# Optimization experiments

Hardware: AMD Instinct MI355X
Metric: run time of the kernel (lower is better)

## Reference

```python
import jax, jax.numpy as jnp
import numpy as np
from jax import lax

B, T, H = 4096, 2048, 32


def setup_inputs() -> dict:
    key = jax.random.key(0)
    ks = jax.random.split(key, 10)
    s = 1.0 / np.sqrt(H)  # PyTorch LSTM/Linear init scale
    x = jax.random.normal(ks[0], (B, T, 1), dtype=jnp.float32)
    lengths = jax.random.randint(ks[1], (B,), 1, T + 1, dtype=jnp.int32)
    u = lambda k, shape, sc: jax.random.uniform(k, shape, jnp.float32, -sc, sc)
    return {
        "x": x,
        "lengths": lengths,
        # backward-direction LSTM weights (only h_n[-1] is used by the head)
        "w_ih": u(ks[2], (4 * H, 1), s),
        "w_hh": u(ks[3], (4 * H, H), s),
        "b_ih": u(ks[4], (4 * H,), s),
        "b_hh": u(ks[5], (4 * H,), s),
        "fc_w": u(ks[6], (64, H), 1.0 / np.sqrt(H)),
        "fc_b": u(ks[7], (64,), 1.0 / np.sqrt(H)),
        "fc2_w": u(ks[8], (1, 64), 1.0 / np.sqrt(64)),
        "fc2_b": u(ks[9], (1,), 1.0 / np.sqrt(64)),
    }


def _backward_lstm_final(x, lengths, w_ih, w_hh, b_ih, b_hh):
    """Final hidden state of the backward direction of a packed BiLSTM.

    The backward direction reads each sequence from t=len-1 down to t=0 with
    zero initial state. Equivalently: scan padded x in reverse time order and
    only update (h, c) where t < length (packed-sequence semantics).
    """
    Bv, Tv, _ = x.shape
    ts = jnp.arange(Tv - 1, -1, -1)                       # reversed time indices
    xs_t = jnp.transpose(x[:, ::-1, :], (1, 0, 2))        # [T, B, 1]
    mask_t = ts[:, None] < lengths[None, :]               # [T, B]

    def step(carry, inp):
        h, c = carry
        xt, m = inp                                        # [B,1], [B]
        gates = xt @ w_ih.T + b_ih + h @ w_hh.T + b_hh     # [B, 4H]
        i, f, g, o = jnp.split(gates, 4, axis=-1)
        i = jax.nn.sigmoid(i)
        f = jax.nn.sigmoid(f)
        g = jnp.tanh(g)
        o = jax.nn.sigmoid(o)
        c_new = f * c + i * g
        h_new = o * jnp.tanh(c_new)
        mm = m[:, None]
        return (jnp.where(mm, h_new, h), jnp.where(mm, c_new, c)), None

    h0 = jnp.zeros((Bv, H), dtype=x.dtype)
    c0 = jnp.zeros((Bv, H), dtype=x.dtype)
    (h_n, _), _ = lax.scan(step, (h0, c0), (xs_t, mask_t))
    return h_n                                             # [B, H]


def reference(x, lengths, w_ih, w_hh, b_ih, b_hh, fc_w, fc_b, fc2_w, fc2_b):
    h_n = _backward_lstm_final(x, lengths, w_ih, w_hh, b_ih, b_hh)
    out = jax.nn.elu(h_n @ fc_w.T + fc_b)                  # [B, 64]
    out = jax.nn.sigmoid(out @ fc2_w.T + fc2_b)            # [B, 1]
    return out
```

## Files before the change

kernel.cpp:

```cpp
#include <hip/hip_runtime.h>

constexpr int BB = 4096;
constexpr int TT = 2048;
constexpr int HH = 32;
constexpr int GE = 16;

typedef float v4f __attribute__((ext_vector_type(4)));
typedef float f32x4 __attribute__((ext_vector_type(4)));
typedef _Float16 f16x8 __attribute__((ext_vector_type(8)));
typedef _Float16 v2h __attribute__((ext_vector_type(2)));
typedef _Float16 v8h __attribute__((ext_vector_type(8)));

__device__ __forceinline__ float fexp2(float x) { return __builtin_amdgcn_exp2f(x); }
__device__ __forceinline__ float frcp(float x)  { return __builtin_amdgcn_rcpf(x); }
__device__ __forceinline__ float fsigmoid(float x) {
    return frcp(1.0f + fexp2(x * -1.4426950408889634f));
}
__device__ __forceinline__ float felu(float x) {
    return x > 0.0f ? x : (fexp2(x * 1.4426950408889634f) - 1.0f);
}

__global__ void sort_by_len_kernel(const int* __restrict__ lengths, int* __restrict__ perm) {
    __shared__ int hist[TT];
    __shared__ int csum[256];
    const int tid = threadIdx.x;
    for (int i = tid; i < TT; i += 256) hist[i] = 0;
    __syncthreads();
    for (int i = tid; i < BB; i += 256) atomicAdd(&hist[TT - lengths[i]], 1);
    __syncthreads();
    const int base = tid * 8;
    int loc[8];
    int s = 0;
#pragma unroll
    for (int j = 0; j < 8; ++j) { loc[j] = hist[base + j]; s += loc[j]; }
    csum[tid] = s;
    __syncthreads();
    for (int off = 1; off < 256; off <<= 1) {
        int v = (tid >= off) ? csum[tid - off] : 0;
        __syncthreads();
        csum[tid] += v;
        __syncthreads();
    }
    int run = csum[tid] - s;
#pragma unroll
    for (int j = 0; j < 8; ++j) { int t = loc[j]; hist[base + j] = run; run += t; }
    __syncthreads();
    for (int i = tid; i < BB; i += 256) {
        int pos = atomicAdd(&hist[TT - lengths[i]], 1);
        perm[pos] = i;
    }
}

__global__ __attribute__((amdgpu_flat_work_group_size(256, 256)))
void lstm_kernel(const float* __restrict__ x, const int* __restrict__ lengths,
                 const float* __restrict__ w_ih, const float* __restrict__ w_hh,
                 const float* __restrict__ b_ih, const float* __restrict__ b_hh,
                 const float* __restrict__ fc_w, const float* __restrict__ fc_b,
                 const float* __restrict__ fc2_w, const float* __restrict__ fc2_b,
                 float* __restrict__ out, const int* __restrict__ perm) {
    __shared__ __align__(16) _Float16 hb[2][GE][40];
    __shared__ __align__(16) float xls[GE][68];
    __shared__ int barr[GE];
    __shared__ int Llds[GE];
    __shared__ int maxLs;

    const int tid  = threadIdx.x;
    const int wv   = tid >> 6;
    const int lane = tid & 63;
    const int lg   = lane >> 4;
    const int e    = lane & 15;

    const int g = blockIdx.x;
    if (tid < GE) {
        const int b = perm ? perm[GE * g + tid] : (GE * g + tid);
        barr[tid] = b;
        Llds[tid] = lengths[b];
    }
    for (int i = tid; i < 2 * GE * 40; i += 256) ((_Float16*)hb)[i] = (_Float16)0.0f;
    __syncthreads();
    if (tid == 0) {
        int m = 0;
        for (int i = 0; i < GE; ++i) m = max(m, Llds[i]);
        maxLs = m;
    }
    __syncthreads();
    const int maxL = maxLs;
    const int Lme  = Llds[e];

    const float NL2E = -1.4426950408889634f;

    const int r = lane & 15;
    const int sgate = r & 3;
    const int qq = r >> 2;
    const float asc = (sgate == 2) ? 2.0f * NL2E : NL2E;
    f16x8 afr[2];
#pragma unroll
    for (int m = 0; m < 2; ++m) {
        const int u = 8 * wv + 2 * qq + m;
        const int wrow = sgate * 32 + u;
        const v4f* wp = reinterpret_cast<const v4f*>(w_hh + wrow * 32 + 8 * lg);
        const v4f wa = wp[0], wb = wp[1];
        afr[m] = (f16x8){(_Float16)(wa.x * asc), (_Float16)(wa.y * asc),
                         (_Float16)(wa.z * asc), (_Float16)(wa.w * asc),
                         (_Float16)(wb.x * asc), (_Float16)(wb.y * asc),
                         (_Float16)(wb.z * asc), (_Float16)(wb.w * asc)};
    }
    float wih_[2][4], bs_[2][4];
#pragma unroll
    for (int m = 0; m < 2; ++m) {
        const int u = 8 * wv + 2 * lg + m;
#pragma unroll
        for (int i = 0; i < 4; ++i) {
            const float scd = (i == 2) ? 2.0f * NL2E : NL2E;
            wih_[m][i] = w_ih[i * 32 + u] * scd;
            bs_[m][i]  = (b_ih[i * 32 + u] + b_hh[i * 32 + u]) * scd;
        }
    }

    float c0 = 0.0f, c1 = 0.0f;
    int p = 0;
    const int hoff = 8 * wv + 2 * lg;

    for (int s = maxL - 1; s >= 0; --s) {
        if (s == maxL - 1 || (s & 63) == 63) {
            const int tb = s & ~63;
            const int es = tid >> 4, j4 = (tid & 15) * 4;
            const float* xp = x + (size_t)barr[es] * TT + tb + j4;
            *reinterpret_cast<v4f*>(&xls[es][j4]) = *reinterpret_cast<const v4f*>(xp);
            __syncthreads();
        }
        const f16x8 bf = *reinterpret_cast<const f16x8*>(&hb[p][e][lg * 8]);
        const float xe = xls[e][s & 63];
        f32x4 C0, C1;
#pragma unroll
        for (int i = 0; i < 4; ++i) {
            C0[i] = fmaf(wih_[0][i], xe, bs_[0][i]);
            C1[i] = fmaf(wih_[1][i], xe, bs_[1][i]);
        }
        const f32x4 D0 = __builtin_amdgcn_mfma_f32_16x16x32_f16(afr[0], bf, C0, 0, 0, 0);
        const f32x4 D1 = __builtin_amdgcn_mfma_f32_16x16x32_f16(afr[1], bf, C1, 0, 0, 0);
        const bool act = (s < Lme);

        float h0, h1;
        {
            const float Ei = fexp2(D0[0]), Ef = fexp2(D0[1]);
            const float Eg = fexp2(D0[2]), Eo = fexp2(D0[3]);
            const float R1 = frcp((1.0f + Ei) * (1.0f + Eg));
            const float ig = (1.0f - Eg) * R1;
            const float R2 = frcp((1.0f + Ef) * (1.0f + Eo));
            const float sf = (1.0f + Eo) * R2;
            const float so = (1.0f + Ef) * R2;
            const float cn = fmaf(sf, c0, ig);
            c0 = act ? cn : c0;
            const float tc = 1.0f - 2.0f * frcp(1.0f + fexp2(c0 * 2.8853900817779268f));
            h0 = act ? (so * tc) : 0.0f;
        }
        {
            const float Ei = fexp2(D1[0]), Ef = fexp2(D1[1]);
            const float Eg = fexp2(D1[2]), Eo = fexp2(D1[3]);
            const float R1 = frcp((1.0f + Ei) * (1.0f + Eg));
            const float ig = (1.0f - Eg) * R1;
            const float R2 = frcp((1.0f + Ef) * (1.0f + Eo));
            const float sf = (1.0f + Eo) * R2;
            const float so = (1.0f + Ef) * R2;
            const float cn = fmaf(sf, c1, ig);
            c1 = act ? cn : c1;
            const float tc = 1.0f - 2.0f * frcp(1.0f + fexp2(c1 * 2.8853900817779268f));
            h1 = act ? (so * tc) : 0.0f;
        }
        const v2h pk = {(_Float16)h0, (_Float16)h1};
        *reinterpret_cast<v2h*>(&hb[p ^ 1][e][hoff]) = pk;
        __syncthreads();
        p ^= 1;
    }

    for (int e2 = 4 * wv; e2 < 4 * wv + 4; ++e2) {
        float hf[32];
        const v8h* hp8 = reinterpret_cast<const v8h*>(&hb[p][e2][0]);
#pragma unroll
        for (int q4 = 0; q4 < 4; ++q4) {
            const v8h hh = hp8[q4];
#pragma unroll
            for (int j = 0; j < 8; ++j) hf[8 * q4 + j] = (float)hh[j];
        }
        float a = fc_b[lane];
        const v4f* fp = reinterpret_cast<const v4f*>(fc_w + lane * 32);
#pragma unroll
        for (int q4 = 0; q4 < 8; ++q4) {
            const v4f f = fp[q4];
            a = fmaf(f.x, hf[4 * q4 + 0], a);
            a = fmaf(f.y, hf[4 * q4 + 1], a);
            a = fmaf(f.z, hf[4 * q4 + 2], a);
            a = fmaf(f.w, hf[4 * q4 + 3], a);
        }
        float partial = felu(a) * fc2_w[lane];
#pragma unroll
        for (int m = 32; m >= 1; m >>= 1) partial += __shfl_xor(partial, m, 64);
        if (lane == 0) out[barr[e2]] = fsigmoid(partial + fc2_b[0]);
    }
}

extern "C" void kernel_launch(void* const* d_in, const int* in_sizes, int n_in,
                              void* d_out, int out_size, void* d_ws, size_t ws_size,
                              hipStream_t stream) {
    const float* x       = (const float*)d_in[0];
    const int*   lengths = (const int*)d_in[1];
    const float* w_ih    = (const float*)d_in[2];
    const float* w_hh    = (const float*)d_in[3];
    const float* b_ih    = (const float*)d_in[4];
    const float* b_hh    = (const float*)d_in[5];
    const float* fc_w    = (const float*)d_in[6];
    const float* fc_b    = (const float*)d_in[7];
    const float* fc2_w   = (const float*)d_in[8];
    const float* fc2_b   = (const float*)d_in[9];
    float* out = (float*)d_out;

    int* perm = nullptr;
    if (ws_size >= (size_t)BB * sizeof(int)) {
        perm = (int*)d_ws;
        hipLaunchKernelGGL(sort_by_len_kernel, dim3(1), dim3(256), 0, stream, lengths, perm);
    }
    hipLaunchKernelGGL(lstm_kernel, dim3(BB / GE), dim3(256), 0, stream,
                       x, lengths, w_ih, w_hh, b_ih, b_hh,
                       fc_w, fc_b, fc2_w, fc2_b, out, perm);
}
```

Before: 676.6 us.

## Split LSTM hidden units across eight waves, one MFMA per wave per step

Doubles the workgroup from 256 to 512 threads so each wave owns four hidden units instead of eight. Each wave issues one MFMA and one set of gate activations per timestep instead of two, which shortens the per-step serial critical path. In exchange, every step's block-wide barrier now synchronises twice as many waves, and each block uses more CUs' worth of wave slots, which lowers how many blocks can run at once.

```diff
diff --git a/kernel.cpp b/kernel.cpp
--- a/kernel.cpp
+++ b/kernel.cpp
@@ -5,10 +5,10 @@
 constexpr int HH = 32;
 constexpr int GE = 16;
 
+typedef float v2f __attribute__((ext_vector_type(2)));
 typedef float v4f __attribute__((ext_vector_type(4)));
 typedef float f32x4 __attribute__((ext_vector_type(4)));
 typedef _Float16 f16x8 __attribute__((ext_vector_type(8)));
-typedef _Float16 v2h __attribute__((ext_vector_type(2)));
 typedef _Float16 v8h __attribute__((ext_vector_type(8)));
 
 __device__ __forceinline__ float fexp2(float x) { return __builtin_amdgcn_exp2f(x); }
@@ -51,7 +51,7 @@
     }
 }
 
-__global__ __attribute__((amdgpu_flat_work_group_size(256, 256)))
+__global__ __attribute__((amdgpu_flat_work_group_size(512, 512)))
 void lstm_kernel(const float* __restrict__ x, const int* __restrict__ lengths,
                  const float* __restrict__ w_ih, const float* __restrict__ w_hh,
                  const float* __restrict__ b_ih, const float* __restrict__ b_hh,
@@ -76,7 +76,7 @@
         barr[tid] = b;
         Llds[tid] = lengths[b];
     }
-    for (int i = tid; i < 2 * GE * 40; i += 256) ((_Float16*)hb)[i] = (_Float16)0.0f;
+    for (int i = tid; i < 2 * GE * 40; i += 512) ((_Float16*)hb)[i] = (_Float16)0.0f;
     __syncthreads();
     if (tid == 0) {
         int m = 0;
@@ -89,92 +89,65 @@
 
     const float NL2E = -1.4426950408889634f;
 
-    const int r = lane & 15;
-    const int sgate = r & 3;
-    const int qq = r >> 2;
-    const float asc = (sgate == 2) ? 2.0f * NL2E : NL2E;
-    f16x8 afr[2];
+    const int r  = lane & 15;
+    const int sg = r & 3;
+    const int ua = 4 * wv + (r >> 2);
+    const float asc = (sg == 2) ? 2.0f * NL2E : NL2E;
+    f16x8 afr;
+    {
+        const v4f* wp = reinterpret_cast<const v4f*>(w_hh + (sg * 32 + ua) * 32 + 8 * lg);
+        const v4f wa = wp[0], wb = wp[1];
+        afr = (f16x8){(_Float16)(wa.x * asc), (_Float16)(wa.y * asc),
+                      (_Float16)(wa.z * asc), (_Float16)(wa.w * asc),
+                      (_Float16)(wb.x * asc), (_Float16)(wb.y * asc),
+                      (_Float16)(wb.z * asc), (_Float16)(wb.w * asc)};
+    }
+    const int ud = 4 * wv + lg;
+    float wih_[4], bs_[4];
 #pragma unroll
-    for (int m = 0; m < 2; ++m) {
-        const int u = 8 * wv + 2 * qq + m;
-        const int wrow = sgate * 32 + u;
-        const v4f* wp = reinterpret_cast<const v4f*>(w_hh + wrow * 32 + 8 * lg);
-        const v4f wa = wp[0], wb = wp[1];
-        afr[m] = (f16x8){(_Float16)(wa.x * asc), (_Float16)(wa.y * asc),
-                         (_Float16)(wa.z * asc), (_Float16)(wa.w * asc),
-                         (_Float16)(wb.x * asc), (_Float16)(wb.y * asc),
-                         (_Float16)(wb.z * asc), (_Float16)(wb.w * asc)};
-    }
-    float wih_[2][4], bs_[2][4];
-#pragma unroll
-    for (int m = 0; m < 2; ++m) {
-        const int u = 8 * wv + 2 * lg + m;
-#pragma unroll
-        for (int i = 0; i < 4; ++i) {
-            const float scd = (i == 2) ? 2.0f * NL2E : NL2E;
-            wih_[m][i] = w_ih[i * 32 + u] * scd;
-            bs_[m][i]  = (b_ih[i * 32 + u] + b_hh[i * 32 + u]) * scd;
-        }
+    for (int i = 0; i < 4; ++i) {
+        const float scd = (i == 2) ? 2.0f * NL2E : NL2E;
+        wih_[i] = w_ih[i * 32 + ud] * scd;
+        bs_[i]  = (b_ih[i * 32 + ud] + b_hh[i * 32 + ud]) * scd;
     }
 
-    float c0 = 0.0f, c1 = 0.0f;
+    float c = 0.0f;
     int p = 0;
-    const int hoff = 8 * wv + 2 * lg;
 
     for (int s = maxL - 1; s >= 0; --s) {
         if (s == maxL - 1 || (s & 63) == 63) {
             const int tb = s & ~63;
-            const int es = tid >> 4, j4 = (tid & 15) * 4;
-            const float* xp = x + (size_t)barr[es] * TT + tb + j4;
-            *reinterpret_cast<v4f*>(&xls[es][j4]) = *reinterpret_cast<const v4f*>(xp);
+            const int es = tid >> 5, j2 = (tid & 31) * 2;
+            const float* xp = x + (size_t)barr[es] * TT + tb + j2;
+            *reinterpret_cast<v2f*>(&xls[es][j2]) = *reinterpret_cast<const v2f*>(xp);
             __syncthreads();
         }
         const f16x8 bf = *reinterpret_cast<const f16x8*>(&hb[p][e][lg * 8]);
         const float xe = xls[e][s & 63];
-        f32x4 C0, C1;
+        f32x4 C;
 #pragma unroll
-        for (int i = 0; i < 4; ++i) {
-            C0[i] = fmaf(wih_[0][i], xe, bs_[0][i]);
-            C1[i] = fmaf(wih_[1][i], xe, bs_[1][i]);
-        }
-        const f32x4 D0 = __builtin_amdgcn_mfma_f32_16x16x32_f16(afr[0], bf, C0, 0, 0, 0);
-        const f32x4 D1 = __builtin_amdgcn_mfma_f32_16x16x32_f16(afr[1], bf, C1, 0, 0, 0);
+        for (int i = 0; i < 4; ++i) C[i] = fmaf(wih_[i], xe, bs_[i]);
+        const f32x4 D = __builtin_amdgcn_mfma_f32_16x16x32_f16(afr, bf, C, 0, 0, 0);
         const bool act = (s < Lme);
 
-        float h0, h1;
-        {
-            const float Ei = fexp2(D0[0]), Ef = fexp2(D0[1]);
-            const float Eg = fexp2(D0[2]), Eo = fexp2(D0[3]);
-            const float R1 = frcp((1.0f + Ei) * (1.0f + Eg));
-            const float ig = (1.0f - Eg) * R1;
-            const float R2 = frcp((1.0f + Ef) * (1.0f + Eo));
-            const float sf = (1.0f + Eo) * R2;
-            const float so = (1.0f + Ef) * R2;
-            const float cn = fmaf(sf, c0, ig);
-            c0 = act ? cn : c0;
-            const float tc = 1.0f - 2.0f * frcp(1.0f + fexp2(c0 * 2.8853900817779268f));
-            h0 = act ? (so * tc) : 0.0f;
-        }
-        {
-            const float Ei = fexp2(D1[0]), Ef = fexp2(D1[1]);
-            const float Eg = fexp2(D1[2]), Eo = fexp2(D1[3]);
-            const float R1 = frcp((1.0f + Ei) * (1.0f + Eg));
-            const float ig = (1.0f - Eg) * R1;
-            const float R2 = frcp((1.0f + Ef) * (1.0f + Eo));
-            const float sf = (1.0f + Eo) * R2;
-            const float so = (1.0f + Ef) * R2;
-            const float cn = fmaf(sf, c1, ig);
-            c1 = act ? cn : c1;
-            const float tc = 1.0f - 2.0f * frcp(1.0f + fexp2(c1 * 2.8853900817779268f));
-            h1 = act ? (so * tc) : 0.0f;
-        }
-        const v2h pk = {(_Float16)h0, (_Float16)h1};
-        *reinterpret_cast<v2h*>(&hb[p ^ 1][e][hoff]) = pk;
+        const float Ei = fexp2(D[0]), Ef = fexp2(D[1]);
+        const float Eg = fexp2(D[2]), Eo = fexp2(D[3]);
+        const float R1 = frcp((1.0f + Ei) * (1.0f + Eg));
+        const float ig = (1.0f - Eg) * R1;
+        const float R2 = frcp((1.0f + Ef) * (1.0f + Eo));
+        const float sf = (1.0f + Eo) * R2;
+        const float so = (1.0f + Ef) * R2;
+        const float cn = fmaf(sf, c, ig);
+        c = act ? cn : c;
+        const float tc = 1.0f - 2.0f * frcp(1.0f + fexp2(c * 2.8853900817779268f));
+        const float hn = act ? (so * tc) : 0.0f;
+
+        hb[p ^ 1][e][ud] = (_Float16)hn;
         __syncthreads();
         p ^= 1;
     }
 
-    for (int e2 = 4 * wv; e2 < 4 * wv + 4; ++e2) {
+    for (int e2 = 2 * wv; e2 < 2 * wv + 2; ++e2) {
         float hf[32];
         const v8h* hp8 = reinterpret_cast<const v8h*>(&hb[p][e2][0]);
 #pragma unroll
@@ -220,7 +193,7 @@
         perm = (int*)d_ws;
         hipLaunchKernelGGL(sort_by_len_kernel, dim3(1), dim3(256), 0, stream, lengths, perm);
     }
-    hipLaunchKernelGGL(lstm_kernel, dim3(BB / GE), dim3(256), 0, stream,
+    hipLaunchKernelGGL(lstm_kernel, dim3(BB / GE), dim3(512), 0, stream,
                        x, lengths, w_ih, w_hh, b_ih, b_hh,
                        fc_w, fc_b, fc2_w, fc2_b, out, perm);
 }
```

Result: faster. 614.6 us (-9.2%).
